# Performance work log

Measured on AMD Instinct MI355X. Metric: run time of the kernel, lower is better.

The kernel has to match this reference:

```python
import jax, jax.numpy as jnp
import numpy as np

S = 2        # subsample_rate
EPS = 1e-5   # BatchNorm eps


def maxpool(x, k):
    B, C, H, W = x.shape
    return x.reshape(B, C, H // k, k, W // k, k).max(axis=(3, 5))


def conv1x1(x, w, b):
    # x: [B,C,H,W], w: [O,C], b: [O]
    return jnp.einsum('bchw,oc->bohw', x, w) + b[None, :, None, None]


def upsample_bilinear_ac(y, s):
    # torch nn.Upsample(mode='bilinear', scale_factor=s, align_corners=True)
    B, C, h, w = y.shape
    H, W = h * s, w * s
    ri = jnp.arange(H, dtype=jnp.float32) * ((h - 1) / (H - 1))
    ci = jnp.arange(W, dtype=jnp.float32) * ((w - 1) / (W - 1))
    r0 = jnp.floor(ri).astype(jnp.int32); r1 = jnp.minimum(r0 + 1, h - 1)
    c0 = jnp.floor(ci).astype(jnp.int32); c1 = jnp.minimum(c0 + 1, w - 1)
    wr = (ri - r0)[None, None, :, None]
    wc = (ci - c0)[None, None, None, :]
    top = y[:, :, r0, :] * (1.0 - wr) + y[:, :, r1, :] * wr
    return top[:, :, :, c0] * (1.0 - wc) + top[:, :, :, c1] * wc


def setup_inputs() -> dict:
    key = jax.random.key(0)
    ks = jax.random.split(key, 12)
    B, C, IC, H, W = 4, 256, 128, 192, 192
    sc = 0.05  # keep attention logits in a sane range
    x = jax.random.normal(ks[0], (B, C, H, W), jnp.float32)
    g_w = jax.random.normal(ks[1], (IC, C), jnp.float32) * sc
    g_b = jax.random.normal(ks[2], (IC,), jnp.float32) * sc
    theta_w = jax.random.normal(ks[3], (IC, C), jnp.float32) * sc
    theta_b = jax.random.normal(ks[4], (IC,), jnp.float32) * sc
    phi_w = jax.random.normal(ks[5], (IC, C), jnp.float32) * sc
    phi_b = jax.random.normal(ks[6], (IC,), jnp.float32) * sc
    W_w = jax.random.normal(ks[7], (C, IC, 3, 3), jnp.float32) * sc
    W_b = jax.random.normal(ks[8], (C,), jnp.float32) * sc
    bn_gamma = jnp.ones((C,), jnp.float32)
    bn_beta = jnp.zeros((C,), jnp.float32)
    bn_mean = jax.random.normal(ks[9], (C,), jnp.float32) * sc
    bn_var = jax.random.uniform(ks[10], (C,), jnp.float32) + 0.5
    return dict(x=x, g_w=g_w, g_b=g_b, theta_w=theta_w, theta_b=theta_b,
                phi_w=phi_w, phi_b=phi_b, W_w=W_w, W_b=W_b,
                bn_gamma=bn_gamma, bn_beta=bn_beta, bn_mean=bn_mean, bn_var=bn_var)


def reference(x, g_w, g_b, theta_w, theta_b, phi_w, phi_b, W_w, W_b,
              bn_gamma, bn_beta, bn_mean, bn_var):
    B, C, H, Wd = x.shape
    IC = g_w.shape[0]
    xp = maxpool(x, S)                               # [B,C,H/S,W/S]
    theta = conv1x1(xp, theta_w, theta_b)            # [B,IC,h,w]
    g = maxpool(conv1x1(xp, g_w, g_b), 2)            # [B,IC,h/2,w/2]
    phi = maxpool(conv1x1(xp, phi_w, phi_b), 2)      # [B,IC,h/2,w/2]
    h, w = theta.shape[2], theta.shape[3]
    th = theta.reshape(B, IC, h * w).transpose(0, 2, 1)   # [B,Nt,IC]
    ph = phi.reshape(B, IC, -1)                           # [B,IC,Np]
    gx = g.reshape(B, IC, -1).transpose(0, 2, 1)          # [B,Np,IC]
    f = jnp.einsum('bnc,bcm->bnm', th, ph)                # [B,Nt,Np]
    a = jax.nn.softmax(f, axis=-1)
    y = jnp.einsum('bnm,bmc->bnc', a, gx)                 # [B,Nt,IC]
    y = y.transpose(0, 2, 1).reshape(B, IC, h, w)
    y = upsample_bilinear_ac(y, S)                        # [B,IC,H,W]
    wy = jax.lax.conv_general_dilated(
        y, W_w, (1, 1), ((1, 1), (1, 1)),
        dimension_numbers=('NCHW', 'OIHW', 'NCHW')) + W_b[None, :, None, None]
    inv = bn_gamma / jnp.sqrt(bn_var + EPS)
    wy = (wy - bn_mean[None, :, None, None]) * inv[None, :, None, None] + bn_beta[None, :, None, None]
    return (wy + x, wy)
```

## Files before the change

kernel.cpp:

```cpp
#include <hip/hip_runtime.h>
#include <hip/hip_bf16.h>
#include <math.h>

#define B_   4
#define C_   256
#define ICH  128
#define H_   192
#define W_   192
#define hs   96
#define ws2  96
#define HW   (hs*ws2)
#define HP   48
#define WP   48
#define NP   (HP*WP)
#define EPSB 1e-5f
#define PADW 194
#define TOT  ((size_t)B_*C_*H_*W_)

#define QB 64
#define KB 64
#define NT (NP/KB)
#define SM_OFF 20.0f

using bf16x8 = __attribute__((ext_vector_type(8))) short;
using f32x4  = __attribute__((ext_vector_type(4))) float;
using f32x16 = __attribute__((ext_vector_type(16))) float;

#define OFF_XPB   ((size_t)0)
#define OFF_THB   ((size_t)4718592)
#define OFF_PHB   ((size_t)7077888)
#define OFF_GBT   ((size_t)7667712)
#define OFF_WB3   ((size_t)8257536)
#define OFF_Y96N  ((size_t)8306688)
#define OFF_ST    ((size_t)13025280)
#define OFF_WT    ((size_t)13025792)
#define OFF_YPAD  ((size_t)13173248)

static __device__ __forceinline__ float b2f(unsigned short u) {
  union { unsigned int i; float f; } c; c.i = (unsigned int)u << 16; return c.f;
}

__global__ __launch_bounds__(256) void k_pool_nhwc(const float* __restrict__ x,
                                                   __hip_bfloat16* __restrict__ xpb) {
  int idx = blockIdx.x * 256 + threadIdx.x;
  int cg = idx & 31;
  int n  = (idx >> 5) % HW;
  int b  = idx / (32 * HW);
  int pi = n / ws2, pj = n % ws2;
  const float* xb = x + (((size_t)b * C_ + cg * 8) * H_ + 2 * pi) * W_ + 2 * pj;
  union { ushort u[8]; uint4 v; } pk;
#pragma unroll
  for (int cc = 0; cc < 8; ++cc) {
    const float* s = xb + (size_t)cc * H_ * W_;
    float v = fmaxf(fmaxf(s[0], s[1]), fmaxf(s[W_], s[W_ + 1]));
    __hip_bfloat16 hv = __float2bfloat16(v);
    pk.u[cc] = *(ushort*)&hv;
  }
  *(uint4*)(xpb + ((size_t)b * HW + n) * C_ + cg * 8) = pk.v;
}

__global__ __launch_bounds__(256) void k_wprep(const float* __restrict__ tw,
                                               const float* __restrict__ gw,
                                               const float* __restrict__ pw,
                                               __hip_bfloat16* __restrict__ wb3) {
  int idx = blockIdx.x * 256 + threadIdx.x;
  int set = idx >> 15; int rem = idx & 32767;
  const float* src = set == 0 ? tw : (set == 1 ? gw : pw);
  wb3[idx] = __float2bfloat16(src[rem]);
}

__global__ __launch_bounds__(256) void k_qkv(
    const __hip_bfloat16* __restrict__ xpb,
    const __hip_bfloat16* __restrict__ wb3,
    const float* __restrict__ tb, const float* __restrict__ gb_,
    const float* __restrict__ pb_,
    __hip_bfloat16* __restrict__ thb,
    __hip_bfloat16* __restrict__ gbt,
    __hip_bfloat16* __restrict__ phb) {
  __shared__ __align__(16) char ldsX[2][192 * 128];
  int t = threadIdx.x;
  int lane = t & 63, li = lane & 15, g4 = lane >> 4;
  int wid = t >> 6;
  int wave_o = wid >> 1, wave_n = wid & 1;
  int i   = blockIdx.x;
  int set = blockIdx.y;
  int b   = blockIdx.z;
  const __hip_bfloat16* wset = wb3 + (size_t)set * 128 * 256;
  const float* bias = set == 0 ? tb : (set == 1 ? gb_ : pb_);
  const size_t xbase = (size_t)b * HW * C_;

  f32x4 acc[4][6];
#pragma unroll
  for (int fo = 0; fo < 4; ++fo)
#pragma unroll
    for (int fq = 0; fq < 6; ++fq) acc[fo][fq] = (f32x4){0.f, 0.f, 0.f, 0.f};

#define STAGEX(step, buf)                                                      \
  for (int e = t; e < 192 * 8; e += 256) {                                     \
    int j = e >> 3, ch = e & 7;                                                \
    int pix = (2 * i + (j & 1)) * ws2 + (j >> 1);                              \
    *(uint4*)(ldsX[buf] + j * 128 + ((ch * 16) ^ ((j & 7) << 4))) =            \
        *(const uint4*)(xpb + xbase + (size_t)pix * C_ + (step) * 64 + ch * 8);\
  }

  STAGEX(0, 0)
  __syncthreads();
  for (int step = 0; step < 4; ++step) {
    int buf = step & 1;
    if (step < 3) { STAGEX(step + 1, buf ^ 1) }
    bf16x8 af[4][2];
#pragma unroll
    for (int fo = 0; fo < 4; ++fo)
#pragma unroll
      for (int ks = 0; ks < 2; ++ks) {
        int o = wave_o * 64 + fo * 16 + li;
        af[fo][ks] = *(const bf16x8*)(wset + (size_t)o * C_ + step * 64 + ks * 32 + g4 * 8);
      }
#pragma unroll
    for (int ks = 0; ks < 2; ++ks)
#pragma unroll
      for (int fq = 0; fq < 6; ++fq) {
        int j = wave_n * 96 + fq * 16 + li;
        bf16x8 bx = *(const bf16x8*)(ldsX[buf] + j * 128 + ((ks * 64 + g4 * 16) ^ ((j & 7) << 4)));
#pragma unroll
        for (int fo = 0; fo < 4; ++fo)
          acc[fo][fq] = __builtin_amdgcn_mfma_f32_16x16x32_bf16(af[fo][ks], bx, acc[fo][fq], 0, 0, 0);
      }
    __syncthreads();
  }

  if (set == 0) {
#pragma unroll
    for (int fo = 0; fo < 4; ++fo) {
      int ob = wave_o * 64 + fo * 16 + g4 * 4;
#pragma unroll
      for (int fq = 0; fq < 6; ++fq) {
        int j = wave_n * 96 + fq * 16 + li;
        int pix = (2 * i + (j & 1)) * ws2 + (j >> 1);
        union { ushort u[4]; uint2 v; } pk;
#pragma unroll
        for (int r = 0; r < 4; ++r) {
          __hip_bfloat16 hv = __float2bfloat16(acc[fo][fq][r] + bias[ob + r]);
          pk.u[r] = *(ushort*)&hv;
        }
        *(uint2*)(thb + ((size_t)b * HW + pix) * ICH + ob) = pk.v;
      }
    }
  } else {
#pragma unroll
    for (int fo = 0; fo < 4; ++fo) {
      int ob = wave_o * 64 + fo * 16 + g4 * 4;
#pragma unroll
      for (int fq = 0; fq < 6; ++fq) {
        float pv[4];
#pragma unroll
        for (int r = 0; r < 4; ++r) {
          float p = acc[fo][fq][r];
          p = fmaxf(p, __shfl_xor(p, 1, 64));
          p = fmaxf(p, __shfl_xor(p, 2, 64));
          pv[r] = p;
        }
        if ((li & 3) == 0) {
          int pc = wave_n * 24 + fq * 4 + (li >> 2);
          int pp = i * WP + pc;
          if (set == 1) {
#pragma unroll
            for (int r = 0; r < 4; ++r)
              gbt[((size_t)b * ICH + ob + r) * NP + pp] = __float2bfloat16(pv[r] + bias[ob + r]);
          } else {
            union { ushort u[4]; uint2 v; } pk;
#pragma unroll
            for (int r = 0; r < 4; ++r) {
              __hip_bfloat16 hv = __float2bfloat16(pv[r] + bias[ob + r]);
              pk.u[r] = *(ushort*)&hv;
            }
            *(uint2*)(phb + ((size_t)b * NP + pp) * ICH + ob) = pk.v;
          }
        }
      }
    }
  }
}

__global__ __launch_bounds__(256) void k_attn_mfma(
    const __hip_bfloat16* __restrict__ thb,
    const __hip_bfloat16* __restrict__ phb,
    const __hip_bfloat16* __restrict__ gbt,
    __hip_bfloat16* __restrict__ y96b) {
  __shared__ __align__(16) char Kl[KB * 256];
  __shared__ __align__(16) char Vl[ICH * KB * 2];
  __shared__ __align__(16) char Pl[4][16 * KB * 2];
  int t = threadIdx.x;
  int lane = t & 63, li = lane & 15, g = lane >> 4;
  int w = t >> 6;
  int flat = blockIdx.x;
  int swz = (flat & 7) * 72 + (flat >> 3);
  int b  = swz / 144;
  int q0 = (swz % 144) * QB;

  bf16x8 aq[4];
  {
    const __hip_bfloat16* qp = thb + ((size_t)b * HW + q0 + w * 16 + li) * ICH + g * 8;
#pragma unroll
    for (int ks = 0; ks < 4; ++ks) aq[ks] = *(const bf16x8*)(qp + ks * 32);
  }

  f32x4 acc_o[8];
#pragma unroll
  for (int ct = 0; ct < 8; ++ct) acc_o[ct] = (f32x4){0.f, 0.f, 0.f, 0.f};
  float l_acc[4] = {0.f, 0.f, 0.f, 0.f};

  char* Pw = (char*)Pl[w];

  for (int kt = 0; kt < NT; ++kt) {
    int m0 = kt * KB;
    __syncthreads();
    for (int e = t; e < KB * 16; e += 256) {
      int mm = e >> 4, ch = e & 15;
      *(uint4*)(Kl + mm * 256 + ((ch * 16) ^ ((mm & 7) << 4))) =
          *(const uint4*)(phb + ((size_t)b * NP + m0 + mm) * ICH + ch * 8);
    }
    for (int e = t; e < ICH * 8; e += 256) {
      int c = e >> 3, ch = e & 7;
      *(uint4*)(Vl + c * 128 + ((ch * 16) ^ ((c & 7) << 4))) =
          *(const uint4*)(gbt + ((size_t)b * ICH + c) * NP + m0 + ch * 8);
    }
    __syncthreads();

    f32x4 s[4];
#pragma unroll
    for (int mt = 0; mt < 4; ++mt) s[mt] = (f32x4){0.f, 0.f, 0.f, 0.f};
#pragma unroll
    for (int mt = 0; mt < 4; ++mt) {
      int m = mt * 16 + li;
#pragma unroll
      for (int ks = 0; ks < 4; ++ks) {
        bf16x8 bk = *(const bf16x8*)(Kl + m * 256 + ((ks * 64 + g * 16) ^ ((li & 7) << 4)));
        s[mt] = __builtin_amdgcn_mfma_f32_16x16x32_bf16(aq[ks], bk, s[mt], 0, 0, 0);
      }
    }

#pragma unroll
    for (int mt = 0; mt < 4; ++mt) {
#pragma unroll
      for (int r = 0; r < 4; ++r) {
        float p = __expf(s[mt][r] - SM_OFF);
        s[mt][r] = p;
        l_acc[r] += p;
      }
    }

#pragma unroll
    for (int mt = 0; mt < 4; ++mt) {
      int m = mt * 16 + li;
#pragma unroll
      for (int r = 0; r < 4; ++r) {
        int ql = g * 4 + r;
        __hip_bfloat16 hv = __float2bfloat16(s[mt][r]);
        *(ushort*)(Pw + ql * 128 + ((m * 2) ^ ((ql & 7) << 4))) = *(ushort*)&hv;
      }
    }

    bf16x8 pa[2];
#pragma unroll
    for (int ks = 0; ks < 2; ++ks)
      pa[ks] = *(const bf16x8*)(Pw + li * 128 + ((ks * 64 + g * 16) ^ ((li & 7) << 4)));
#pragma unroll
    for (int ct = 0; ct < 8; ++ct) {
      int c = ct * 16 + li;
#pragma unroll
      for (int ks = 0; ks < 2; ++ks) {
        bf16x8 bv = *(const bf16x8*)(Vl + c * 128 + ((ks * 64 + g * 16) ^ ((c & 7) << 4)));
        acc_o[ct] = __builtin_amdgcn_mfma_f32_16x16x32_bf16(pa[ks], bv, acc_o[ct], 0, 0, 0);
      }
    }
  }

  float inv[4];
#pragma unroll
  for (int r = 0; r < 4; ++r) {
    float l = l_acc[r];
    l += __shfl_xor(l, 1, 64);
    l += __shfl_xor(l, 2, 64);
    l += __shfl_xor(l, 4, 64);
    l += __shfl_xor(l, 8, 64);
    inv[r] = 1.f / l;
  }
  __hip_bfloat16* ob = y96b + ((size_t)b * HW + q0 + w * 16 + g * 4) * ICH + li;
#pragma unroll
  for (int r = 0; r < 4; ++r)
#pragma unroll
    for (int ct = 0; ct < 8; ++ct)
      ob[(size_t)r * ICH + ct * 16] = __float2bfloat16(acc_o[ct][r] * inv[r]);
}

__global__ __launch_bounds__(256) void k_up_pad(const __hip_bfloat16* __restrict__ y96b,
                                                __hip_bfloat16* __restrict__ ypad) {
  int idx = blockIdx.x * 256 + threadIdx.x;
  int pc  = idx % PADW;
  int r2  = idx / PADW;
  int ic8 = r2 & 15;
  int r3  = r2 >> 4;
  int pr  = r3 % PADW;
  int b   = r3 / PADW;
  __hip_bfloat16* dst = ypad + (size_t)idx * 8;
  if (pr == 0 || pr == PADW - 1 || pc == 0 || pc == PADW - 1) {
    uint2 z = {0, 0};
    *(uint2*)dst = z;
    *(uint2*)(dst + 4) = z;
    return;
  }
  int p = pr - 1, q = pc - 1;
  const float sc = 95.0f / 191.0f;
  float ri = p * sc, ci = q * sc;
  int r0 = (int)ri; int r1 = min(r0 + 1, hs - 1); float wr = ri - r0;
  int c0 = (int)ci; int c1 = min(c0 + 1, ws2 - 1); float wc = ci - c0;
  const __hip_bfloat16* base = y96b + (size_t)b * HW * ICH + ic8 * 8;
  union { ushort u[4]; uint2 v; } a, bb, cc, dd, pk;
  a.v  = *(const uint2*)(base + ((size_t)r0 * ws2 + c0) * ICH);
  bb.v = *(const uint2*)(base + ((size_t)r0 * ws2 + c1) * ICH);
  cc.v = *(const uint2*)(base + ((size_t)r1 * ws2 + c0) * ICH);
  dd.v = *(const uint2*)(base + ((size_t)r1 * ws2 + c1) * ICH);
  union { ushort u[4]; uint2 v; } a2, bb2, cc2, dd2, pk2;
  a2.v  = *(const uint2*)(base + ((size_t)r0 * ws2 + c0) * ICH + 4);
  bb2.v = *(const uint2*)(base + ((size_t)r0 * ws2 + c1) * ICH + 4);
  cc2.v = *(const uint2*)(base + ((size_t)r1 * ws2 + c0) * ICH + 4);
  dd2.v = *(const uint2*)(base + ((size_t)r1 * ws2 + c1) * ICH + 4);
#pragma unroll
  for (int j = 0; j < 4; ++j) {
    float top = b2f(a.u[j]) * (1.f - wr) + b2f(cc.u[j]) * wr;
    float bot = b2f(bb.u[j]) * (1.f - wr) + b2f(dd.u[j]) * wr;
    float v = top * (1.f - wc) + bot * wc;
    __hip_bfloat16 hv = __float2bfloat16(v);
    pk.u[j] = *(ushort*)&hv;
    float top2 = b2f(a2.u[j]) * (1.f - wr) + b2f(cc2.u[j]) * wr;
    float bot2 = b2f(bb2.u[j]) * (1.f - wr) + b2f(dd2.u[j]) * wr;
    float v2 = top2 * (1.f - wc) + bot2 * wc;
    __hip_bfloat16 hv2 = __float2bfloat16(v2);
    pk2.u[j] = *(ushort*)&hv2;
  }
  *(uint2*)dst = pk.v;
  *(uint2*)(dst + 4) = pk2.v;
}

__global__ __launch_bounds__(256) void k_wt(const float* __restrict__ Ww,
                                            __hip_bfloat16* __restrict__ Wt) {
  int idx = blockIdx.x * 256 + threadIdx.x;
  int lo  = idx & 7;
  int o   = (idx >> 3) & 255;
  int ic8 = (idx >> 11) & 15;
  int tap = idx >> 15;
  int ic  = ic8 * 8 + lo;
  Wt[idx] = __float2bfloat16(Ww[(size_t)o * (ICH * 9) + ic * 9 + tap]);
}

__global__ __launch_bounds__(256) void k_bnprep(const float* __restrict__ Wb,
                                                const float* __restrict__ bg,
                                                const float* __restrict__ bb,
                                                const float* __restrict__ bm,
                                                const float* __restrict__ bv,
                                                float* __restrict__ ST) {
  int o = threadIdx.x;
  float sc = bg[o] * rsqrtf(bv[o] + EPSB);
  ST[o] = sc;
  ST[256 + o] = (Wb[o] - bm[o]) * sc + bb[o];
}

#define ABY 12288
#define BBY 6208
#define BUF (ABY + BBY)
__global__ __launch_bounds__(256) void k_conv3_mfma(
    const __hip_bfloat16* __restrict__ ypad,
    const __hip_bfloat16* __restrict__ Wt,
    const float* __restrict__ ST,
    const float* __restrict__ x,
    float* __restrict__ out) {
  __shared__ __align__(16) char ldsM[2 * BUF];
  int t = threadIdx.x;
  int lane = t & 63;
  int l31 = lane & 31, h = lane >> 5;
  int wid = t >> 6;
  int wave_o = wid >> 1, wave_q = wid & 1;

  int flat = blockIdx.x;
  int swz = (flat & 7) * 192 + (flat >> 3);
  int p  = swz % H_;
  int zz = swz / H_;
  int b  = zz >> 1;
  int o0 = (zz & 1) * 128;

  f32x16 acc[2][3];
#pragma unroll
  for (int i = 0; i < 2; ++i)
#pragma unroll
    for (int j = 0; j < 3; ++j)
#pragma unroll
      for (int r = 0; r < 16; ++r) acc[i][j][r] = 0.f;

#define STG(s_, buf_)                                                           \
  {                                                                             \
    int kh_ = (s_) >> 3, icE_ = (s_) & 7;                                       \
    char* base_ = ldsM + (buf_) * BUF;                                          \
    const __hip_bfloat16* wb_ = Wt;                                             \
    _Pragma("unroll")                                                           \
    for (int rr = 0; rr < 3; ++rr) {                                            \
      int e = rr * 256 + t;                                                     \
      int tap_ = e >> 8, ch_ = (e >> 7) & 1, o_ = e & 127;                      \
      size_t gsl = (((size_t)(kh_ * 3 + tap_) * 16 + icE_ * 2 + ch_) * 256 + o0 + o_) * 8; \
      __builtin_amdgcn_global_load_lds(                                         \
          (const __attribute__((address_space(1))) void*)(wb_ + gsl),           \
          (__attribute__((address_space(3))) void*)(base_ + (rr * 256 + (t & 192)) * 16), \
          16, 0, 0);                                                            \
    }                                                                           \
    const __hip_bfloat16* br_ = ypad;                                           \
    _Pragma("unroll")                                                           \
    for (int rr = 0; rr < 2; ++rr) {                                            \
      int e = rr * 256 + t;                                                     \
      if (e < 388) {                                                            \
        int ch_ = (e >= 194) ? 1 : 0;                                           \
        int col_ = e - ch_ * 194;                                               \
        size_t gsl = (((size_t)(b * PADW + p + kh_) * 16 + icE_ * 2 + ch_) * PADW + col_) * 8; \
        __builtin_amdgcn_global_load_lds(                                       \
            (const __attribute__((address_space(1))) void*)(br_ + gsl),         \
            (__attribute__((address_space(3))) void*)(base_ + ABY + (rr * 256 + (t & 192)) * 16), \
            16, 0, 0);                                                          \
      }                                                                         \
    }                                                                           \
  }

  STG(0, 0)
  __syncthreads();
  for (int s = 0; s < 24; ++s) {
    if (s < 23) { STG(s + 1, (s + 1) & 1) }
    const char* Ab = ldsM + (s & 1) * BUF;
    const char* Bb = Ab + ABY;
#pragma unroll
    for (int kw = 0; kw < 3; ++kw) {
      bf16x8 afr[2], bfr[3];
#pragma unroll
      for (int fo = 0; fo < 2; ++fo)
        afr[fo] = *(const bf16x8*)(Ab + (kw * 256 + h * 128 + wave_o * 64 + fo * 32 + l31) * 16);
#pragma unroll
      for (int fq = 0; fq < 3; ++fq)
        bfr[fq] = *(const bf16x8*)(Bb + (h * 194 + wave_q * 96 + fq * 32 + l31 + kw) * 16);
#pragma unroll
      for (int fo = 0; fo < 2; ++fo)
#pragma unroll
        for (int fq = 0; fq < 3; ++fq)
          acc[fo][fq] = __builtin_amdgcn_mfma_f32_32x32x16_bf16(
              afr[fo], bfr[fq], acc[fo][fq], 0, 0, 0);
    }
    __syncthreads();
  }

#pragma unroll
  for (int fo = 0; fo < 2; ++fo) {
#pragma unroll
    for (int fq = 0; fq < 3; ++fq) {
#pragma unroll
      for (int r = 0; r < 16; ++r) {
        int o = o0 + wave_o * 64 + fo * 32 + (r & 3) + 8 * (r >> 2) + 4 * h;
        int q = wave_q * 96 + fq * 32 + l31;
        size_t oi = (((size_t)b * C_ + o) * H_ + p) * W_ + q;
        float val = acc[fo][fq][r] * ST[o] + ST[256 + o];
        out[TOT + oi] = val;
        out[oi] = val + x[oi];
      }
    }
  }
}

extern "C" void kernel_launch(void* const* d_in, const int* in_sizes, int n_in,
                              void* d_out, int out_size, void* d_ws, size_t ws_size,
                              hipStream_t stream) {
  const float* x    = (const float*)d_in[0];
  const float* g_w  = (const float*)d_in[1];
  const float* g_b  = (const float*)d_in[2];
  const float* th_w = (const float*)d_in[3];
  const float* th_b = (const float*)d_in[4];
  const float* ph_w = (const float*)d_in[5];
  const float* ph_b = (const float*)d_in[6];
  const float* W_w  = (const float*)d_in[7];
  const float* W_b  = (const float*)d_in[8];
  const float* bn_g = (const float*)d_in[9];
  const float* bn_b = (const float*)d_in[10];
  const float* bn_m = (const float*)d_in[11];
  const float* bn_v = (const float*)d_in[12];
  float* out = (float*)d_out;
  float* ws  = (float*)d_ws;

  __hip_bfloat16* xpb = (__hip_bfloat16*)(ws + OFF_XPB);
  __hip_bfloat16* thb = (__hip_bfloat16*)(ws + OFF_THB);
  __hip_bfloat16* phb = (__hip_bfloat16*)(ws + OFF_PHB);
  __hip_bfloat16* gbt = (__hip_bfloat16*)(ws + OFF_GBT);
  __hip_bfloat16* wb3 = (__hip_bfloat16*)(ws + OFF_WB3);
  __hip_bfloat16* y96b = (__hip_bfloat16*)(ws + OFF_Y96N);
  float* ST   = ws + OFF_ST;
  __hip_bfloat16* Wt   = (__hip_bfloat16*)(ws + OFF_WT);
  __hip_bfloat16* ypad = (__hip_bfloat16*)(ws + OFF_YPAD);

  k_pool_nhwc<<<(B_ * HW * 32) / 256, 256, 0, stream>>>(x, xpb);
  k_wprep<<<(3 * 128 * 256) / 256, 256, 0, stream>>>(th_w, g_w, ph_w, wb3);
  k_qkv<<<dim3(HP, 3, B_), 256, 0, stream>>>(xpb, wb3, th_b, g_b, ph_b, thb, gbt, phb);
  k_attn_mfma<<<dim3(B_ * (HW / QB)), 256, 0, stream>>>(thb, phb, gbt, y96b);
  k_up_pad<<<(B_ * PADW * 16 * PADW) / 256, 256, 0, stream>>>(y96b, ypad);
  k_wt<<<(9 * 16 * 256 * 8) / 256, 256, 0, stream>>>(W_w, Wt);
  k_bnprep<<<1, 256, 0, stream>>>(W_b, bn_g, bn_b, bn_m, bn_v, ST);
  k_conv3_mfma<<<dim3(H_ * B_ * 2), 256, 0, stream>>>(ypad, Wt, ST, x, out);
}
```

Before: 459.2 us.

## Double-buffer attention K/V tiles via async global-to-LDS loads with fine-grained waitcnt

The attention kernel now stages K and V tiles with global_load_lds into two LDS buffers, prefetching the next tile while computing on the current one. The swizzle is moved into the global source address. The conv3 kernel replaces __syncthreads with partial vmcnt waits, so one stage's loads stay in flight while the previous stage is consumed. Conv3 also drops the bounds branch by clamping (which issues duplicate loads) and grows the B buffer. Together these aim to hide global-memory latency, at the cost of more LDS and reliance on exact vmcnt counts for correctness.

Measured after the change: 490.1 us. +6.7%, slower.

```diff
diff --git a/kernel.cpp b/kernel.cpp
--- a/kernel.cpp
+++ b/kernel.cpp
@@ -187,8 +187,8 @@
     const __hip_bfloat16* __restrict__ phb,
     const __hip_bfloat16* __restrict__ gbt,
     __hip_bfloat16* __restrict__ y96b) {
-  __shared__ __align__(16) char Kl[KB * 256];
-  __shared__ __align__(16) char Vl[ICH * KB * 2];
+  __shared__ __align__(16) char Kl[2][KB * 256];
+  __shared__ __align__(16) char Vl[2][ICH * KB * 2];
   __shared__ __align__(16) char Pl[4][16 * KB * 2];
   int t = threadIdx.x;
   int lane = t & 63, li = lane & 15, g = lane >> 4;
@@ -212,20 +212,39 @@
 
   char* Pw = (char*)Pl[w];
 
+#define STGKV(kt_, buf_)                                                        \
+  {                                                                             \
+    int m0_ = (kt_) * KB;                                                       \
+    _Pragma("unroll")                                                           \
+    for (int rr = 0; rr < 4; ++rr) {                                            \
+      int e = rr * 256 + t;                                                     \
+      int mm = e >> 4, ch = (e & 15) ^ (mm & 7);                                \
+      __builtin_amdgcn_global_load_lds(                                         \
+          (const __attribute__((address_space(1))) void*)(phb + ((size_t)b * NP + m0_ + mm) * ICH + ch * 8), \
+          (__attribute__((address_space(3))) void*)(Kl[buf_] + (rr * 256 + (t & 192)) * 16), \
+          16, 0, 0);                                                            \
+    }                                                                           \
+    _Pragma("unroll")                                                           \
+    for (int rr = 0; rr < 4; ++rr) {                                            \
+      int e = rr * 256 + t;                                                     \
+      int c = e >> 3, ch = (e & 7) ^ (c & 7);                                   \
+      __builtin_amdgcn_global_load_lds(                                         \
+          (const __attribute__((address_space(1))) void*)(gbt + ((size_t)b * ICH + c) * NP + m0_ + ch * 8), \
+          (__attribute__((address_space(3))) void*)(Vl[buf_] + (rr * 256 + (t & 192)) * 16), \
+          16, 0, 0);                                                            \
+    }                                                                           \
+  }
+
+  STGKV(0, 0)
   for (int kt = 0; kt < NT; ++kt) {
-    int m0 = kt * KB;
-    __syncthreads();
-    for (int e = t; e < KB * 16; e += 256) {
-      int mm = e >> 4, ch = e & 15;
-      *(uint4*)(Kl + mm * 256 + ((ch * 16) ^ ((mm & 7) << 4))) =
-          *(const uint4*)(phb + ((size_t)b * NP + m0 + mm) * ICH + ch * 8);
-    }
-    for (int e = t; e < ICH * 8; e += 256) {
-      int c = e >> 3, ch = e & 7;
-      *(uint4*)(Vl + c * 128 + ((ch * 16) ^ ((c & 7) << 4))) =
-          *(const uint4*)(gbt + ((size_t)b * ICH + c) * NP + m0 + ch * 8);
-    }
-    __syncthreads();
+    int buf = kt & 1;
+    if (kt < NT - 1) {
+      STGKV(kt + 1, buf ^ 1)
+      asm volatile("s_waitcnt vmcnt(8)" ::: "memory");
+    } else {
+      asm volatile("s_waitcnt vmcnt(0)" ::: "memory");
+    }
+    __builtin_amdgcn_s_barrier();
 
     f32x4 s[4];
 #pragma unroll
@@ -235,7 +254,7 @@
       int m = mt * 16 + li;
 #pragma unroll
       for (int ks = 0; ks < 4; ++ks) {
-        bf16x8 bk = *(const bf16x8*)(Kl + m * 256 + ((ks * 64 + g * 16) ^ ((li & 7) << 4)));
+        bf16x8 bk = *(const bf16x8*)(Kl[buf] + m * 256 + ((ks * 64 + g * 16) ^ ((li & 7) << 4)));
         s[mt] = __builtin_amdgcn_mfma_f32_16x16x32_bf16(aq[ks], bk, s[mt], 0, 0, 0);
       }
     }
@@ -270,10 +289,11 @@
       int c = ct * 16 + li;
 #pragma unroll
       for (int ks = 0; ks < 2; ++ks) {
-        bf16x8 bv = *(const bf16x8*)(Vl + c * 128 + ((ks * 64 + g * 16) ^ ((c & 7) << 4)));
+        bf16x8 bv = *(const bf16x8*)(Vl[buf] + c * 128 + ((ks * 64 + g * 16) ^ ((c & 7) << 4)));
         acc_o[ct] = __builtin_amdgcn_mfma_f32_16x16x32_bf16(pa[ks], bv, acc_o[ct], 0, 0, 0);
       }
     }
+    __builtin_amdgcn_s_barrier();
   }
 
   float inv[4];
@@ -367,7 +387,7 @@
 }
 
 #define ABY 12288
-#define BBY 6208
+#define BBY 8192
 #define BUF (ABY + BBY)
 __global__ __launch_bounds__(256) void k_conv3_mfma(
     const __hip_bfloat16* __restrict__ ypad,
@@ -401,37 +421,39 @@
   {                                                                             \
     int kh_ = (s_) >> 3, icE_ = (s_) & 7;                                       \
     char* base_ = ldsM + (buf_) * BUF;                                          \
-    const __hip_bfloat16* wb_ = Wt;                                             \
     _Pragma("unroll")                                                           \
     for (int rr = 0; rr < 3; ++rr) {                                            \
       int e = rr * 256 + t;                                                     \
       int tap_ = e >> 8, ch_ = (e >> 7) & 1, o_ = e & 127;                      \
       size_t gsl = (((size_t)(kh_ * 3 + tap_) * 16 + icE_ * 2 + ch_) * 256 + o0 + o_) * 8; \
       __builtin_amdgcn_global_load_lds(                                         \
-          (const __attribute__((address_space(1))) void*)(wb_ + gsl),           \
+          (const __attribute__((address_space(1))) void*)(Wt + gsl),            \
           (__attribute__((address_space(3))) void*)(base_ + (rr * 256 + (t & 192)) * 16), \
           16, 0, 0);                                                            \
     }                                                                           \
-    const __hip_bfloat16* br_ = ypad;                                           \
     _Pragma("unroll")                                                           \
     for (int rr = 0; rr < 2; ++rr) {                                            \
       int e = rr * 256 + t;                                                     \
-      if (e < 388) {                                                            \
-        int ch_ = (e >= 194) ? 1 : 0;                                           \
-        int col_ = e - ch_ * 194;                                               \
-        size_t gsl = (((size_t)(b * PADW + p + kh_) * 16 + icE_ * 2 + ch_) * PADW + col_) * 8; \
-        __builtin_amdgcn_global_load_lds(                                       \
-            (const __attribute__((address_space(1))) void*)(br_ + gsl),         \
-            (__attribute__((address_space(3))) void*)(base_ + ABY + (rr * 256 + (t & 192)) * 16), \
-            16, 0, 0);                                                          \
-      }                                                                         \
+      int ec = e < 388 ? e : 387;                                               \
+      int ch_ = (ec >= 194) ? 1 : 0;                                            \
+      int col_ = ec - ch_ * 194;                                                \
+      size_t gsl = (((size_t)(b * PADW + p + kh_) * 16 + icE_ * 2 + ch_) * PADW + col_) * 8; \
+      __builtin_amdgcn_global_load_lds(                                         \
+          (const __attribute__((address_space(1))) void*)(ypad + gsl),          \
+          (__attribute__((address_space(3))) void*)(base_ + ABY + (rr * 256 + (t & 192)) * 16), \
+          16, 0, 0);                                                            \
     }                                                                           \
   }
 
   STG(0, 0)
-  __syncthreads();
   for (int s = 0; s < 24; ++s) {
-    if (s < 23) { STG(s + 1, (s + 1) & 1) }
+    if (s < 23) {
+      STG(s + 1, (s + 1) & 1)
+      asm volatile("s_waitcnt vmcnt(5)" ::: "memory");
+    } else {
+      asm volatile("s_waitcnt vmcnt(0)" ::: "memory");
+    }
+    __builtin_amdgcn_s_barrier();
     const char* Ab = ldsM + (s & 1) * BUF;
     const char* Bb = Ab + ABY;
 #pragma unroll
@@ -450,7 +472,7 @@
           acc[fo][fq] = __builtin_amdgcn_mfma_f32_32x32x16_bf16(
               afr[fo], bfr[fq], acc[fo][fq], 0, 0, 0);
     }
-    __syncthreads();
+    __builtin_amdgcn_s_barrier();
   }
 
 #pragma unroll
```
